# Optimization experiments

Hardware: AMD Instinct MI355X
Metric: run time of the kernel (lower is better)

Reference implementation:

```python
import jax, jax.numpy as jnp
import numpy as np

N, E, G = 50000, 400000, 64
F_IN, HID, HEADS, GF, NCLS = 16, 128, 4, 10, 6


def _init(k, shape, fan):
    return jax.random.normal(k, shape, jnp.float32) * (1.0 / np.sqrt(fan))


def setup_inputs() -> dict:
    key = jax.random.key(0)
    ks = jax.random.split(key, 16)
    x = jax.random.normal(ks[0], (N, F_IN), jnp.float32)
    edge_index = jax.random.randint(ks[1], (2, E), 0, N)
    batch = jnp.sort(jax.random.randint(ks[2], (N,), 0, G))
    graph_feat = jax.random.normal(ks[3], (G, GF), jnp.float32)
    # GATConv 1: in=16 -> heads=4, out=128, concat
    W1 = _init(ks[4], (F_IN, HEADS * HID), F_IN)
    att_src1 = _init(ks[5], (HEADS, HID), HID)
    att_dst1 = _init(ks[6], (HEADS, HID), HID)
    b1 = jnp.zeros((HEADS * HID,), jnp.float32)
    # GATConv 2: in=512 -> heads=1, out=128, mean (concat=False)
    W2 = _init(ks[7], (HEADS * HID, HID), HEADS * HID)
    att_src2 = _init(ks[8], (1, HID), HID)
    att_dst2 = _init(ks[9], (1, HID), HID)
    b2 = jnp.zeros((HID,), jnp.float32)
    # graph_proj MLP 10->32->32
    Wg1 = _init(ks[10], (GF, 32), GF); bg1 = jnp.zeros((32,), jnp.float32)
    Wg2 = _init(ks[11], (32, 32), 32); bg2 = jnp.zeros((32,), jnp.float32)
    # classifier 160->128->6
    Wc1 = _init(ks[12], (HID + 32, 128), HID + 32); bc1 = jnp.zeros((128,), jnp.float32)
    Wc2 = _init(ks[13], (128, NCLS), 128); bc2 = jnp.zeros((NCLS,), jnp.float32)
    return dict(x=x, edge_index=edge_index, batch=batch, graph_feat=graph_feat,
                W1=W1, att_src1=att_src1, att_dst1=att_dst1, b1=b1,
                W2=W2, att_src2=att_src2, att_dst2=att_dst2, b2=b2,
                Wg1=Wg1, bg1=bg1, Wg2=Wg2, bg2=bg2,
                Wc1=Wc1, bc1=bc1, Wc2=Wc2, bc2=bc2)


def gat_layer(x, W, att_src, att_dst, bias, src, dst, n_nodes, heads, out_dim, concat):
    # Linear transform: [N, H, C]
    h = (x @ W).reshape(n_nodes, heads, out_dim)
    a_src = jnp.einsum('nhc,hc->nh', h, att_src)  # [N,H]
    a_dst = jnp.einsum('nhc,hc->nh', h, att_dst)  # [N,H]
    e = jax.nn.leaky_relu(a_src[src] + a_dst[dst], 0.2)  # [Etot,H]
    # segment softmax over edges grouped by dst (self-loops ensure nonempty)
    m = jax.ops.segment_max(e, dst, num_segments=n_nodes)
    ex = jnp.exp(e - m[dst])
    denom = jax.ops.segment_sum(ex, dst, num_segments=n_nodes)
    alpha = ex / denom[dst]  # [Etot,H]
    out = jax.ops.segment_sum(alpha[:, :, None] * h[src], dst, num_segments=n_nodes)  # [N,H,C]
    if concat:
        out = out.reshape(n_nodes, heads * out_dim)
    else:
        out = out.mean(axis=1)
    return out + bias


def reference(x, edge_index, batch, graph_feat,
              W1, att_src1, att_dst1, b1,
              W2, att_src2, att_dst2, b2,
              Wg1, bg1, Wg2, bg2, Wc1, bc1, Wc2, bc2):
    n = x.shape[0]
    loops = jnp.arange(n, dtype=edge_index.dtype)
    src = jnp.concatenate([edge_index[0], loops])
    dst = jnp.concatenate([edge_index[1], loops])
    h = jax.nn.elu(gat_layer(x, W1, att_src1, att_dst1, b1, src, dst, n, HEADS, HID, True))
    h = jax.nn.elu(gat_layer(h, W2, att_src2, att_dst2, b2, src, dst, n, 1, HID, False))
    # global mean pool over graphs
    g = graph_feat.shape[0]
    sums = jax.ops.segment_sum(h, batch, num_segments=g)
    counts = jax.ops.segment_sum(jnp.ones((n, 1), h.dtype), batch, num_segments=g)
    pooled = sums / jnp.maximum(counts, 1.0)
    gf = jax.nn.relu(graph_feat @ Wg1 + bg1) @ Wg2 + bg2
    z = jnp.concatenate([pooled, gf], axis=1)
    z = jax.nn.relu(z @ Wc1 + bc1)
    return z @ Wc2 + bc2
```

## Files before the change

kernel.cpp:

```cpp
#include <hip/hip_runtime.h>
#include <hip/hip_bf16.h>

#define NN 50000
#define EE 400000
#define GG 64
#define CAP 48
#define GB1 782

typedef unsigned short u16;
typedef unsigned char u8;
typedef long long i64;
typedef __attribute__((ext_vector_type(8))) short bf16x8;
typedef __attribute__((ext_vector_type(4))) float f32x4;
typedef __attribute__((ext_vector_type(2))) float f32x2;

__device__ __forceinline__ float b2f(u16 u) {
    unsigned int x = ((unsigned int)u) << 16;
    return __uint_as_float(x);
}
__device__ __forceinline__ u16 f2b(float f) {
    unsigned int x = __float_as_uint(f);
    unsigned int r = x + 0x7fffu + ((x >> 16) & 1u);
    return (u16)(r >> 16);
}
__device__ __forceinline__ u8 f2fp8(float f) {
    return (u8)(__builtin_amdgcn_cvt_pk_fp8_f32(f, f, 0, false) & 0xFF);
}
__device__ __forceinline__ f32x2 fp8x2_f32(unsigned int v, bool hi) {
    return hi ? __builtin_amdgcn_cvt_pk_f32_fp8(v, true)
              : __builtin_amdgcn_cvt_pk_f32_fp8(v, false);
}
__device__ __forceinline__ float wred_sum(float v) {
    #pragma unroll
    for (int o = 32; o; o >>= 1) v += __shfl_xor(v, o, 64);
    return v;
}
__device__ __forceinline__ float lrelu(float v) { return v > 0.f ? v : 0.2f * v; }

__global__ void k_prep(const int* __restrict__ batch, int* __restrict__ deg,
                       int* __restrict__ col, int* __restrict__ gstart,
                       const float* __restrict__ W1, const float* __restrict__ as1,
                       const float* __restrict__ ad1, u16* __restrict__ W1p,
                       const float* __restrict__ W2, u8* __restrict__ W2p,
                       float* __restrict__ pooled) {
    __shared__ float asw[16][8];
    int b = blockIdx.x, t = threadIdx.x;
    if (b < 196) {
        int n = b * 256 + t;
        if (n < NN) { deg[n] = 1; col[(size_t)n * CAP] = n; }
    } else if (b == 196) {
        if (t <= GG) {
            int lo = 0, hi = NN;
            while (lo < hi) {
                int mid = (lo + hi) >> 1;
                if (batch[mid] < t) lo = mid + 1; else hi = mid;
            }
            gstart[t] = lo;
        }
    } else if (b < 453) {
        int idx = (b - 197) * 256 + t;
        int j = idx & 7;
        int l = (idx >> 3) & 63;
        int ct = idx >> 9;
        int c = ct >> 3, tt = ct & 7;
        int k = c * 32 + (l >> 4) * 8 + j;
        int n = tt * 16 + (l & 15);
        W2p[idx] = f2fp8(W2[k * 128 + n]);
    } else if (b == 453) {
        int pair = t >> 1, half = t & 1;
        int k = pair >> 3, h = pair & 7;
        int hd = h & 3;
        const float* att = (h >= 4) ? ad1 : as1;
        float s = 0.f;
        int c0 = half * 64;
        for (int c = c0; c < c0 + 64; c++)
            s += W1[k * 512 + hd * 128 + c] * att[hd * 128 + c];
        s += __shfl_xor(s, 1, 64);
        if (half == 0) asw[k][h] = s;
        __syncthreads();
        for (int idx = t; idx < 33 * 64 * 8; idx += 256) {
            int j = idx & 7, l = (idx >> 3) & 63, tt = idx >> 9;
            int quad = l >> 4, m = l & 15;
            int k2 = quad * 8 + j;
            float v = 0.f;
            if (k2 < 16) {
                if (tt < 32) v = W1[k2 * 512 + tt * 16 + m];
                else if (m < 8) v = asw[k2][m];
            }
            W1p[idx] = f2b(v);
        }
    } else {
        for (int i = t; i < GG * 128; i += 256) pooled[i] = 0.f;
    }
}

__global__ __launch_bounds__(256) void k_ge(
    const float* __restrict__ x, const u16* __restrict__ W1p,
    u8* __restrict__ h1, float* __restrict__ a_src1, float* __restrict__ a_dst1,
    const int* __restrict__ ei, int* __restrict__ deg, int* __restrict__ col) {
    int tid = threadIdx.x;
    if (blockIdx.x >= GB1) {
        int e = (blockIdx.x - GB1) * 256 + tid;
        if (e < EE) {
            int s = ei[e];
            int d = ei[EE + e];
            int slot = atomicAdd(&deg[d], 1);
            if (slot < CAP) col[(size_t)d * CAP + slot] = s;
        }
        return;
    }
    int wave = tid >> 6, l = tid & 63;
    int quad = l >> 4, m = l & 15;
    int row0 = blockIdx.x * 64 + wave * 16;
    int arow = row0 + m;
    int arow_c = arow < NN ? arow : (NN - 1);
    bf16x8 af;
    if (quad < 2) {
        const float* xp = x + arow_c * 16 + quad * 8;
        float4 x0 = *(const float4*)(xp);
        float4 x1 = *(const float4*)(xp + 4);
        u16 tmp[8] = {f2b(x0.x), f2b(x0.y), f2b(x0.z), f2b(x0.w),
                      f2b(x1.x), f2b(x1.y), f2b(x1.z), f2b(x1.w)};
        af = *(bf16x8*)tmp;
    } else {
        af = (bf16x8){0, 0, 0, 0, 0, 0, 0, 0};
    }
    const u16* bp = W1p + l * 8;
    f32x4 acc[33];
    #pragma unroll
    for (int tt = 0; tt < 33; tt++) acc[tt] = (f32x4){0.f, 0.f, 0.f, 0.f};
    #pragma unroll
    for (int tt = 0; tt < 33; tt++) {
        bf16x8 bf = *(const bf16x8*)(bp + (size_t)tt * 512);
        acc[tt] = __builtin_amdgcn_mfma_f32_16x16x32_bf16(af, bf, acc[tt], 0, 0, 0);
    }
    #pragma unroll
    for (int r = 0; r < 4; r++) {
        int row = row0 + quad * 4 + r;
        if (row >= NN) continue;
        unsigned int d[8];
        #pragma unroll
        for (int dd = 0; dd < 8; dd++) {
            unsigned int w = __builtin_amdgcn_cvt_pk_fp8_f32(acc[4 * dd][r], acc[4 * dd + 1][r], 0, false);
            w = __builtin_amdgcn_cvt_pk_fp8_f32(acc[4 * dd + 2][r], acc[4 * dd + 3][r], w, true);
            d[dd] = w;
        }
        uint4 v0; v0.x = d[0]; v0.y = d[1]; v0.z = d[2]; v0.w = d[3];
        uint4 v1; v1.x = d[4]; v1.y = d[5]; v1.z = d[6]; v1.w = d[7];
        *(uint4*)(h1 + (size_t)row * 512 + m * 32) = v0;
        *(uint4*)(h1 + (size_t)row * 512 + m * 32 + 16) = v1;
        float v = acc[32][r];
        if (m < 4) a_src1[row * 4 + m] = v;
        else if (m < 8) a_dst1[row * 4 + (m - 4)] = v;
    }
}

__global__ __launch_bounds__(256) void k_agg1(
    const int* __restrict__ deg, const int* __restrict__ col,
    const float* __restrict__ a_src1, const float* __restrict__ a_dst1,
    const u8* __restrict__ h1, const float* __restrict__ b1,
    u8* __restrict__ h2pre) {
    __shared__ float alphaS[4][64][4];
    int t = threadIdx.x;
    int wave = t >> 6, l = t & 63;
    int n = blockIdx.x * 4 + wave;
    if (n >= NN) return;
    int dg = min(deg[n], CAP);
    int sl = (l < dg) ? col[(size_t)n * CAP + l] : 0;
    float4 ad = *(const float4*)(a_dst1 + n * 4);
    float4 as = *(const float4*)(a_src1 + (size_t)sl * 4);
    float4 e;
    e.x = __expf(lrelu(as.x + ad.x)); e.y = __expf(lrelu(as.y + ad.y));
    e.z = __expf(lrelu(as.z + ad.z)); e.w = __expf(lrelu(as.w + ad.w));
    if (l >= dg) e = (float4){0.f, 0.f, 0.f, 0.f};
    float4 inv;
    inv.x = 1.0f / wred_sum(e.x);
    inv.y = 1.0f / wred_sum(e.y);
    inv.z = 1.0f / wred_sum(e.z);
    inv.w = 1.0f / wred_sum(e.w);
    {
        float4 a4;
        a4.x = e.x * inv.x; a4.y = e.y * inv.y;
        a4.z = e.z * inv.z; a4.w = e.w * inv.w;
        *(float4*)&alphaS[wave][l][0] = a4;
    }
    int g = l >> 4, m = l & 15;
    const u8* hb = h1 + m * 32 + g * 8;
    f32x2 acc[4] = {{0.f, 0.f}, {0.f, 0.f}, {0.f, 0.f}, {0.f, 0.f}};
    int iters = (dg + 3) >> 2;
    for (int j = 0; j < iters; j++) {
        int e0 = 4 * j, e1 = 4 * j + 1, e2 = 4 * j + 2, e3 = 4 * j + 3;
        int s0 = __shfl(sl, e0), s1 = __shfl(sl, e1);
        int s2 = __shfl(sl, e2), s3 = __shfl(sl, e3);
        float a0 = alphaS[wave][e0][g], a1 = alphaS[wave][e1][g];
        float a2 = alphaS[wave][e2][g], a3 = alphaS[wave][e3][g];
        uint2 u0 = *(const uint2*)(hb + (size_t)s0 * 512);
        uint2 u1 = *(const uint2*)(hb + (size_t)s1 * 512);
        uint2 u2 = *(const uint2*)(hb + (size_t)s2 * 512);
        uint2 u3 = *(const uint2*)(hb + (size_t)s3 * 512);
        acc[0] += a0 * fp8x2_f32(u0.x, false);
        acc[1] += a0 * fp8x2_f32(u0.x, true);
        acc[2] += a0 * fp8x2_f32(u0.y, false);
        acc[3] += a0 * fp8x2_f32(u0.y, true);
        acc[0] += a1 * fp8x2_f32(u1.x, false);
        acc[1] += a1 * fp8x2_f32(u1.x, true);
        acc[2] += a1 * fp8x2_f32(u1.y, false);
        acc[3] += a1 * fp8x2_f32(u1.y, true);
        acc[0] += a2 * fp8x2_f32(u2.x, false);
        acc[1] += a2 * fp8x2_f32(u2.x, true);
        acc[2] += a2 * fp8x2_f32(u2.y, false);
        acc[3] += a2 * fp8x2_f32(u2.y, true);
        acc[0] += a3 * fp8x2_f32(u3.x, false);
        acc[1] += a3 * fp8x2_f32(u3.x, true);
        acc[2] += a3 * fp8x2_f32(u3.y, false);
        acc[3] += a3 * fp8x2_f32(u3.y, true);
    }
    float av[8] = {acc[0].x, acc[0].y, acc[1].x, acc[1].y,
                   acc[2].x, acc[2].y, acc[3].x, acc[3].y};
    u8* op = h2pre + (size_t)n * 512 + 128 * g + m;
    const float* bb = b1 + 128 * g + m;
    #pragma unroll
    for (int j = 0; j < 8; j++) {
        float v = av[j] + bb[16 * j];
        v = v > 0.f ? v : __expf(v) - 1.0f;
        op[16 * j] = f2fp8(v);
    }
}

__global__ __launch_bounds__(256) void k_gemm2(
    const u8* __restrict__ h2pre, const u8* __restrict__ W2p,
    const float* __restrict__ as2, const float* __restrict__ ad2,
    u8* __restrict__ hL2, float* __restrict__ a_src2, float* __restrict__ a_dst2) {
    int t = threadIdx.x;
    int wave = t >> 6, l = t & 63;
    int quad = l >> 4, m = l & 15;
    int row0 = blockIdx.x * 64 + wave * 16;
    int arow = row0 + m;
    int arow_c = arow < NN ? arow : (NN - 1);
    const u8* aptr = h2pre + (size_t)arow_c * 512 + quad * 8;
    const u8* bptr = W2p + l * 8;
    f32x4 acc[8];
    #pragma unroll
    for (int tt = 0; tt < 8; tt++) acc[tt] = (f32x4){0.f, 0.f, 0.f, 0.f};
    for (int c = 0; c < 16; c++) {
        i64 af = *(const i64*)(aptr + c * 32);
        #pragma unroll
        for (int tt = 0; tt < 8; tt++) {
            i64 bf = *(const i64*)(bptr + (size_t)(c * 8 + tt) * 512);
            acc[tt] = __builtin_amdgcn_mfma_f32_16x16x32_fp8_fp8(af, bf, acc[tt], 0, 0, 0);
        }
    }
    float asv[8], adv[8];
    #pragma unroll
    for (int tt = 0; tt < 8; tt++) {
        int colc = tt * 16 + m;
        asv[tt] = as2[colc];
        adv[tt] = ad2[colc];
    }
    #pragma unroll
    for (int r = 0; r < 4; r++) {
        int row = row0 + quad * 4 + r;
        bool ok = row < NN;
        float rs = 0.f, rd = 0.f;
        #pragma unroll
        for (int tt = 0; tt < 8; tt++) {
            float v = acc[tt][r];
            if (ok) hL2[(size_t)row * 128 + tt * 16 + m] = f2fp8(v);
            rs += v * asv[tt];
            rd += v * adv[tt];
        }
        #pragma unroll
        for (int o = 1; o < 16; o <<= 1) {
            rs += __shfl_xor(rs, o, 64);
            rd += __shfl_xor(rd, o, 64);
        }
        if (ok && m == 0) { a_src2[row] = rs; a_dst2[row] = rd; }
    }
}

__global__ __launch_bounds__(256) void k_agg2(
    const int* __restrict__ deg, const int* __restrict__ col,
    const float* __restrict__ a_src2, const float* __restrict__ a_dst2,
    const u8* __restrict__ hL2, const float* __restrict__ b2v,
    const int* __restrict__ batch, float* __restrict__ pooled) {
    __shared__ float red[4][128];
    __shared__ int gS[4];
    int t = threadIdx.x;
    int wave = t >> 6, l = t & 63;
    int n = blockIdx.x * 4 + wave;
    if (n >= NN) return;
    int dg = min(deg[n], CAP);
    int sl = (l < dg) ? col[(size_t)n * CAP + l] : 0;
    float ad = a_dst2[n];
    float e = (l < dg) ? __expf(lrelu(a_src2[sl] + ad)) : 0.f;
    float inv = 1.0f / wred_sum(e);
    float al = e * inv;
    f32x2 acc = {0.f, 0.f};
    const u8* hb = hL2 + l * 2;
    int iters = (dg + 3) >> 2;
    for (int j = 0; j < iters; j++) {
        int e0 = 4 * j, e1 = 4 * j + 1, e2 = 4 * j + 2, e3 = 4 * j + 3;
        int s0 = __shfl(sl, e0), s1 = __shfl(sl, e1);
        int s2 = __shfl(sl, e2), s3 = __shfl(sl, e3);
        float a0 = __shfl(al, e0), a1 = __shfl(al, e1);
        float a2 = __shfl(al, e2), a3 = __shfl(al, e3);
        unsigned int u0 = *(const u16*)(hb + (size_t)s0 * 128);
        unsigned int u1 = *(const u16*)(hb + (size_t)s1 * 128);
        unsigned int u2 = *(const u16*)(hb + (size_t)s2 * 128);
        unsigned int u3 = *(const u16*)(hb + (size_t)s3 * 128);
        acc += a0 * fp8x2_f32(u0, false);
        acc += a1 * fp8x2_f32(u1, false);
        acc += a2 * fp8x2_f32(u2, false);
        acc += a3 * fp8x2_f32(u3, false);
    }
    float o0 = acc.x + b2v[2 * l];     o0 = o0 > 0.f ? o0 : __expf(o0) - 1.0f;
    float o1 = acc.y + b2v[2 * l + 1]; o1 = o1 > 0.f ? o1 : __expf(o1) - 1.0f;
    red[wave][2 * l] = o0;
    red[wave][2 * l + 1] = o1;
    if (l == 0) gS[wave] = batch[n];
    __syncthreads();
    if (t < 128) {
        int g0 = gS[0];
        if (gS[1] == g0 && gS[2] == g0 && gS[3] == g0) {
            float s = red[0][t] + red[1][t] + red[2][t] + red[3][t];
            atomicAdd(&pooled[g0 * 128 + t], s);
        } else {
            #pragma unroll
            for (int w = 0; w < 4; w++)
                atomicAdd(&pooled[gS[w] * 128 + t], red[w][t]);
        }
    }
}

__global__ __launch_bounds__(128) void k_head(
    const int* __restrict__ gstart, const float* __restrict__ pooled,
    const float* __restrict__ gfeat,
    const float* __restrict__ Wg1, const float* __restrict__ bg1,
    const float* __restrict__ Wg2, const float* __restrict__ bg2,
    const float* __restrict__ Wc1, const float* __restrict__ bc1,
    const float* __restrict__ Wc2, const float* __restrict__ bc2,
    float* __restrict__ out) {
    __shared__ float z[160];
    __shared__ float hg[32];
    __shared__ float c1b[128];
    int g = blockIdx.x, t = threadIdx.x;
    float cntf = (float)(gstart[g + 1] - gstart[g]);
    z[t] = pooled[g * 128 + t] / fmaxf(cntf, 1.0f);
    if (t < 32) {
        float a = bg1[t];
        for (int i = 0; i < 10; i++) a += gfeat[g * 10 + i] * Wg1[i * 32 + t];
        hg[t] = fmaxf(a, 0.f);
    }
    __syncthreads();
    if (t < 32) {
        float a = bg2[t];
        for (int i = 0; i < 32; i++) a += hg[i] * Wg2[i * 32 + t];
        z[128 + t] = a;
    }
    __syncthreads();
    float a = bc1[t];
    for (int i = 0; i < 160; i++) a += z[i] * Wc1[i * 128 + t];
    c1b[t] = fmaxf(a, 0.f);
    __syncthreads();
    if (t < 6) {
        float o = bc2[t];
        for (int i = 0; i < 128; i++) o += c1b[i] * Wc2[i * 6 + t];
        out[g * 6 + t] = o;
    }
}

extern "C" void kernel_launch(void* const* d_in, const int* in_sizes, int n_in,
                              void* d_out, int out_size, void* d_ws, size_t ws_size,
                              hipStream_t stream) {
    const float* x     = (const float*)d_in[0];
    const int*   ei    = (const int*)d_in[1];
    const int*   batch = (const int*)d_in[2];
    const float* gfeat = (const float*)d_in[3];
    const float* W1    = (const float*)d_in[4];
    const float* as1   = (const float*)d_in[5];
    const float* ad1   = (const float*)d_in[6];
    const float* b1    = (const float*)d_in[7];
    const float* W2    = (const float*)d_in[8];
    const float* as2   = (const float*)d_in[9];
    const float* ad2   = (const float*)d_in[10];
    const float* b2    = (const float*)d_in[11];
    const float* Wg1   = (const float*)d_in[12];
    const float* bg1   = (const float*)d_in[13];
    const float* Wg2   = (const float*)d_in[14];
    const float* bg2   = (const float*)d_in[15];
    const float* Wc1   = (const float*)d_in[16];
    const float* bc1   = (const float*)d_in[17];
    const float* Wc2   = (const float*)d_in[18];
    const float* bc2   = (const float*)d_in[19];
    float* out = (float*)d_out;

    size_t off = 0;
    char* base = (char*)d_ws;
    auto take = [&](size_t nbytes) -> char* {
        char* p = base + off;
        off = (off + nbytes + 255) & ~(size_t)255;
        return p;
    };
    u8*    h1     = (u8*)take((size_t)NN * 512);
    u8*    h2pre  = (u8*)take((size_t)NN * 512);
    u8*    hL2    = (u8*)take((size_t)NN * 128);
    float* a_src1 = (float*)take((size_t)NN * 4 * 4);
    float* a_dst1 = (float*)take((size_t)NN * 4 * 4);
    float* a_src2 = (float*)take((size_t)NN * 4);
    float* a_dst2 = (float*)take((size_t)NN * 4);
    int*   deg    = (int*)take((size_t)NN * 4);
    int*   col    = (int*)take((size_t)NN * CAP * 4);
    float* pooled = (float*)take(GG * 128 * 4);
    int*   gstart = (int*)take((GG + 1) * 4);
    u8*    W2p    = (u8*)take((size_t)512 * 128);
    u16*   W1p    = (u16*)take((size_t)33 * 64 * 8 * 2);
    (void)ws_size; (void)in_sizes; (void)n_in; (void)out_size;

    k_prep<<<455, 256, 0, stream>>>(batch, deg, col, gstart, W1, as1, ad1, W1p,
                                    W2, W2p, pooled);
    k_ge<<<GB1 + (EE + 255) / 256, 256, 0, stream>>>(x, W1p, h1, a_src1, a_dst1,
                                                     ei, deg, col);
    k_agg1<<<(NN + 3) / 4, 256, 0, stream>>>(deg, col, a_src1, a_dst1, h1, b1, h2pre);
    k_gemm2<<<(NN + 63) / 64, 256, 0, stream>>>(h2pre, W2p, as2, ad2, hL2, a_src2, a_dst2);
    k_agg2<<<(NN + 3) / 4, 256, 0, stream>>>(deg, col, a_src2, a_dst2, hL2, b2,
                                             batch, pooled);
    k_head<<<GG, 128, 0, stream>>>(gstart, pooled, gfeat, Wg1, bg1, Wg2, bg2,
                                   Wc1, bc1, Wc2, bc2, out);
}
```

Before: 262.3 us.

## Permute hidden channel layout to allow packed fp8 stores; split edge kernel

Stores the intermediate h2pre and hL2 activations in a permuted channel order. Each lane can then pack eight fp8 values with cvt_pk_fp8_f32 and write a single 8-byte store instead of eight scattered byte stores. W2 packing and the agg2 bias/pooling indexing are remapped to match the new order. It also splits the fused GEMM1 plus edge-bucketing kernel into two separate launches, which adds a launch and loses the overlap between the two.

```diff
diff --git a/kernel.cpp b/kernel.cpp
--- a/kernel.cpp
+++ b/kernel.cpp
@@ -5,7 +5,6 @@
 #define EE 400000
 #define GG 64
 #define CAP 48
-#define GB1 782
 
 typedef unsigned short u16;
 typedef unsigned char u8;
@@ -63,9 +62,11 @@
         int l = (idx >> 3) & 63;
         int ct = idx >> 9;
         int c = ct >> 3, tt = ct & 7;
-        int k = c * 32 + (l >> 4) * 8 + j;
+        int p = c * 32 + (l >> 4) * 8 + j;
+        int lp = p >> 3, jp = p & 7;
+        int chan = 128 * (lp >> 4) + 16 * jp + (lp & 15);
         int n = tt * 16 + (l & 15);
-        W2p[idx] = f2fp8(W2[k * 128 + n]);
+        W2p[idx] = f2fp8(W2[chan * 128 + n]);
     } else if (b == 453) {
         int pair = t >> 1, half = t & 1;
         int k = pair >> 3, h = pair & 7;
@@ -94,21 +95,21 @@
     }
 }
 
-__global__ __launch_bounds__(256) void k_ge(
+__global__ void k_edges(const int* __restrict__ ei, int* __restrict__ deg,
+                        int* __restrict__ col) {
+    int e = blockIdx.x * 256 + threadIdx.x;
+    if (e < EE) {
+        int s = ei[e];
+        int d = ei[EE + e];
+        int slot = atomicAdd(&deg[d], 1);
+        if (slot < CAP) col[(size_t)d * CAP + slot] = s;
+    }
+}
+
+__global__ __launch_bounds__(256) void k_gemm1(
     const float* __restrict__ x, const u16* __restrict__ W1p,
-    u8* __restrict__ h1, float* __restrict__ a_src1, float* __restrict__ a_dst1,
-    const int* __restrict__ ei, int* __restrict__ deg, int* __restrict__ col) {
+    u8* __restrict__ h1, float* __restrict__ a_src1, float* __restrict__ a_dst1) {
     int tid = threadIdx.x;
-    if (blockIdx.x >= GB1) {
-        int e = (blockIdx.x - GB1) * 256 + tid;
-        if (e < EE) {
-            int s = ei[e];
-            int d = ei[EE + e];
-            int slot = atomicAdd(&deg[d], 1);
-            if (slot < CAP) col[(size_t)d * CAP + slot] = s;
-        }
-        return;
-    }
     int wave = tid >> 6, l = tid & 63;
     int quad = l >> 4, m = l & 15;
     int row0 = blockIdx.x * 64 + wave * 16;
@@ -217,14 +218,19 @@
     }
     float av[8] = {acc[0].x, acc[0].y, acc[1].x, acc[1].y,
                    acc[2].x, acc[2].y, acc[3].x, acc[3].y};
-    u8* op = h2pre + (size_t)n * 512 + 128 * g + m;
     const float* bb = b1 + 128 * g + m;
+    float v[8];
     #pragma unroll
     for (int j = 0; j < 8; j++) {
-        float v = av[j] + bb[16 * j];
-        v = v > 0.f ? v : __expf(v) - 1.0f;
-        op[16 * j] = f2fp8(v);
-    }
+        float w = av[j] + bb[16 * j];
+        v[j] = w > 0.f ? w : __expf(w) - 1.0f;
+    }
+    unsigned int d0 = __builtin_amdgcn_cvt_pk_fp8_f32(v[0], v[1], 0, false);
+    d0 = __builtin_amdgcn_cvt_pk_fp8_f32(v[2], v[3], d0, true);
+    unsigned int d1 = __builtin_amdgcn_cvt_pk_fp8_f32(v[4], v[5], 0, false);
+    d1 = __builtin_amdgcn_cvt_pk_fp8_f32(v[6], v[7], d1, true);
+    uint2 ov; ov.x = d0; ov.y = d1;
+    *(uint2*)(h2pre + (size_t)n * 512 + l * 8) = ov;
 }
 
 __global__ __launch_bounds__(256) void k_gemm2(
@@ -265,9 +271,16 @@
         #pragma unroll
         for (int tt = 0; tt < 8; tt++) {
             float v = acc[tt][r];
-            if (ok) hL2[(size_t)row * 128 + tt * 16 + m] = f2fp8(v);
             rs += v * asv[tt];
             rd += v * adv[tt];
+        }
+        if (ok) {
+            unsigned int d0 = __builtin_amdgcn_cvt_pk_fp8_f32(acc[0][r], acc[1][r], 0, false);
+            d0 = __builtin_amdgcn_cvt_pk_fp8_f32(acc[2][r], acc[3][r], d0, true);
+            unsigned int d1 = __builtin_amdgcn_cvt_pk_fp8_f32(acc[4][r], acc[5][r], 0, false);
+            d1 = __builtin_amdgcn_cvt_pk_fp8_f32(acc[6][r], acc[7][r], d1, true);
+            uint2 ov; ov.x = d0; ov.y = d1;
+            *(uint2*)(hL2 + (size_t)row * 128 + m * 8) = ov;
         }
         #pragma unroll
         for (int o = 1; o < 16; o <<= 1) {
@@ -313,10 +326,12 @@
         acc += a2 * fp8x2_f32(u2, false);
         acc += a3 * fp8x2_f32(u3, false);
     }
-    float o0 = acc.x + b2v[2 * l];     o0 = o0 > 0.f ? o0 : __expf(o0) - 1.0f;
-    float o1 = acc.y + b2v[2 * l + 1]; o1 = o1 > 0.f ? o1 : __expf(o1) - 1.0f;
-    red[wave][2 * l] = o0;
-    red[wave][2 * l + 1] = o1;
+    int c0 = ((2 * l) & 7) * 16 + (l >> 2);
+    int c1 = c0 + 16;
+    float o0 = acc.x + b2v[c0]; o0 = o0 > 0.f ? o0 : __expf(o0) - 1.0f;
+    float o1 = acc.y + b2v[c1]; o1 = o1 > 0.f ? o1 : __expf(o1) - 1.0f;
+    red[wave][c0] = o0;
+    red[wave][c1] = o1;
     if (l == 0) gS[wave] = batch[n];
     __syncthreads();
     if (t < 128) {
@@ -418,8 +433,8 @@
 
     k_prep<<<455, 256, 0, stream>>>(batch, deg, col, gstart, W1, as1, ad1, W1p,
                                     W2, W2p, pooled);
-    k_ge<<<GB1 + (EE + 255) / 256, 256, 0, stream>>>(x, W1p, h1, a_src1, a_dst1,
-                                                     ei, deg, col);
+    k_edges<<<(EE + 255) / 256, 256, 0, stream>>>(ei, deg, col);
+    k_gemm1<<<(NN + 63) / 64, 256, 0, stream>>>(x, W1p, h1, a_src1, a_dst1);
     k_agg1<<<(NN + 3) / 4, 256, 0, stream>>>(deg, col, a_src1, a_dst1, h1, b1, h2pre);
     k_gemm2<<<(NN + 63) / 64, 256, 0, stream>>>(h2pre, W2p, as2, ad2, hL2, a_src2, a_dst2);
     k_agg2<<<(NN + 3) / 4, 256, 0, stream>>>(deg, col, a_src2, a_dst2, hL2, b2,
```

Result: faster. 255.3 us (-2.7%).
